# Optimization experiments

Hardware: AMD Instinct MI355X
Metric: run time of the kernel (lower is better)

## Reference

```python
import jax, jax.numpy as jnp
import numpy as np

N_RAYS = 8192
N_SAMPLES = 512  # hardcoded n_samples=512 in source
HID = 32
BOOSTER = 1.0


def setup_inputs() -> dict:
    key = jax.random.key(0)
    ks = jax.random.split(key, 8)
    # camera placed outside the box at z=-3, rays pointing toward +z into the aabb
    o = jnp.array([0.0, 0.0, -3.0]) + 0.05 * jax.random.normal(ks[0], (N_RAYS, 3))
    dxy = 0.5 * (2.0 * jax.random.uniform(ks[1], (N_RAYS, 2)) - 1.0)
    d = jnp.concatenate([dxy, jnp.ones((N_RAYS, 1))], axis=-1)  # unnormalized world dirs
    aabb = jnp.array([[-1.0, -1.0, -1.0], [1.0, 1.0, 1.0]])
    u = jax.random.uniform(ks[2], (N_RAYS, N_SAMPLES))  # stratified jitter
    W1 = 0.5 * jax.random.normal(ks[3], (3, HID))
    b1 = jnp.zeros((HID,))
    Wc = 0.2 * jax.random.normal(ks[4], (HID, 3))
    bc = jnp.zeros((3,))
    Wd = 0.2 * jax.random.normal(ks[5], (HID, 1))
    bd = jnp.zeros((1,))
    return dict(o=o, d=d, aabb=aabb, u=u, W1=W1, b1=b1, Wc=Wc, bc=bc, Wd=Wd, bd=bd)


def reference(o, d, aabb, u, W1, b1, Wc, bc, Wd, bd):
    # --- intersect_aabb (slab test) ---
    t1 = (aabb[0] - o) / d
    t2 = (aabb[1] - o) / d
    tnear = jnp.maximum(jnp.max(jnp.minimum(t1, t2), axis=-1), 0.0)  # [N]
    tfar = jnp.min(jnp.maximum(t1, t2), axis=-1)                      # [N]
    active = tnear < tfar                                             # [N] active_mask
    dnorm = jnp.linalg.norm(d, axis=-1, keepdims=True)                # [N,1]

    # --- sample_ray_step_stratified: T bins in [tnear, tfar], jittered ---
    idx = jnp.arange(N_SAMPLES, dtype=o.dtype)
    ts = tnear[:, None] + (tfar - tnear)[:, None] * (idx[None, :] + u) / N_SAMPLES  # [N,T]

    # --- query radiance field at xyz = o + d*ts ---
    xyz = o[:, None, :] + d[:, None, :] * ts[..., None]               # [N,T,3]
    ndc = 2.0 * (xyz - aabb[0]) / (aabb[1] - aabb[0]) - 1.0           # box-normalized
    inbox = jnp.all(jnp.abs(ndc) <= 1.0, axis=-1)                     # BoundsFilter.test
    h = jax.nn.relu(ndc @ W1 + b1)                                    # [N,T,HID]
    color = jax.nn.sigmoid(h @ Wc + bc)                               # [N,T,3]
    density = jax.nn.softplus(h @ Wd + bd)[..., 0]                    # [N,T]
    # masked scatter-back: out-of-box samples contribute zero
    density = jnp.where(inbox, density, 0.0)
    color = jnp.where(inbox[..., None], color, 0.0)

    # --- integrate_timesteps: alpha compositing with cumulative transmittance ---
    t_ext = jnp.concatenate([ts, (tfar + BOOSTER)[:, None]], axis=-1)
    delta = (t_ext[:, 1:] - t_ext[:, :-1]) * dnorm                    # [N,T]
    sd = density * delta
    trans = jnp.exp(-jnp.concatenate([jnp.zeros_like(sd[:, :1]), jnp.cumsum(sd[:, :-1], axis=-1)], axis=-1))
    w = trans * (1.0 - jnp.exp(-sd))                                  # weights [N,T]

    out_color = jnp.einsum('nt,ntc->nc', w, color)                    # color_map
    out_alpha = jnp.sum(w, axis=-1, keepdims=True)                    # alpha_map

    act = active[:, None].astype(o.dtype)                             # scatter to active rays only
    return jnp.concatenate([out_color * act, out_alpha * act], axis=-1)  # [N,4]
```

## Files before the change

### kernel.cpp

```cpp
#include <hip/hip_runtime.h>
#include <math.h>

#define NRAYS 8192
#define NS 512
#define HID 32
#define SPL 8

typedef float f32x2 __attribute__((ext_vector_type(2)));

__global__ __launch_bounds__(256) void render_kernel(
    const float* __restrict__ o_, const float* __restrict__ d_,
    const float* __restrict__ aabb, const float* __restrict__ u_,
    const float* __restrict__ W1, const float* __restrict__ b1,
    const float* __restrict__ Wc, const float* __restrict__ bc,
    const float* __restrict__ Wd, const float* __restrict__ bd,
    float* __restrict__ out)
{
    __shared__ float wsh[272];
    const int tid = threadIdx.x;

    if (tid < HID) {
        const int j = tid, p = j >> 1, h = j & 1;
        float* base = wsh + p * 16;
        base[0 + h]  = W1[0 * HID + j];
        base[2 + h]  = W1[1 * HID + j];
        base[4 + h]  = W1[2 * HID + j];
        base[6 + h]  = b1[j];
        base[8 + h]  = Wc[j * 3 + 0];
        base[10 + h] = Wc[j * 3 + 1];
        base[12 + h] = Wc[j * 3 + 2];
        base[14 + h] = Wd[j];
    } else if (tid == HID) {
        wsh[256] = bc[0]; wsh[257] = bc[1]; wsh[258] = bc[2]; wsh[259] = bd[0];
    }
    __syncthreads();

    const int lane = tid & 63;
    const int ray  = (blockIdx.x << 2) + (tid >> 6);
    if (ray >= NRAYS) return;

    const float ox = o_[ray * 3 + 0], oy = o_[ray * 3 + 1], oz = o_[ray * 3 + 2];
    const float dx = d_[ray * 3 + 0], dy = d_[ray * 3 + 1], dz = d_[ray * 3 + 2];
    const float lox = aabb[0], loy = aabb[1], loz = aabb[2];
    const float hix = aabb[3], hiy = aabb[4], hiz = aabb[5];

    float t1 = (lox - ox) / dx, t2 = (hix - ox) / dx;
    float tnear = fminf(t1, t2), tfar = fmaxf(t1, t2);
    t1 = (loy - oy) / dy; t2 = (hiy - oy) / dy;
    tnear = fmaxf(tnear, fminf(t1, t2)); tfar = fminf(tfar, fmaxf(t1, t2));
    t1 = (loz - oz) / dz; t2 = (hiz - oz) / dz;
    tnear = fmaxf(tnear, fminf(t1, t2)); tfar = fminf(tfar, fmaxf(t1, t2));
    tnear = fmaxf(tnear, 0.0f);

    float4 res = make_float4(0.0f, 0.0f, 0.0f, 0.0f);

    if (tnear < tfar) {
        const float dnorm = sqrtf(dx * dx + dy * dy + dz * dz);
        const float dt = (tfar - tnear) * (1.0f / (float)NS);
        const float sx = 2.0f / (hix - lox);
        const float sy = 2.0f / (hiy - loy);
        const float sz = 2.0f / (hiz - loz);
        const float bc0 = wsh[256], bc1 = wsh[257], bc2 = wsh[258], bd0 = wsh[259];

        const int base_t = lane * SPL;
        const float* __restrict__ urow = u_ + (size_t)ray * NS + base_t;
        const float4 uaq = *reinterpret_cast<const float4*>(urow);
        const float4 ubq = *reinterpret_cast<const float4*>(urow + 4);
        float us[9];
        us[0] = uaq.x; us[1] = uaq.y; us[2] = uaq.z; us[3] = uaq.w;
        us[4] = ubq.x; us[5] = ubq.y; us[6] = ubq.z; us[7] = ubq.w;
        us[8] = __shfl_down(uaq.x, 1);

        f32x2 nx2[SPL], ny2[SPL], nz2[SPL];
        float delta[SPL];
        #pragma unroll
        for (int s = 0; s < SPL; ++s) {
            const int t = base_t + s;
            const float ts = fmaf(dt, (float)t + us[s], tnear);
            float dl;
            if (t == NS - 1) dl = (tfar + 1.0f) - ts;
            else             dl = dt * (1.0f + us[s + 1] - us[s]);
            delta[s] = dl * dnorm;
            const float px = fmaf(dx, ts, ox);
            const float py = fmaf(dy, ts, oy);
            const float pz = fmaf(dz, ts, oz);
            const float nx = (px - lox) * sx - 1.0f;
            const float ny = (py - loy) * sy - 1.0f;
            const float nz = (pz - loz) * sz - 1.0f;
            nx2[s] = (f32x2){nx, nx};
            ny2[s] = (f32x2){ny, ny};
            nz2[s] = (f32x2){nz, nz};
        }

        f32x2 cr2[SPL], cg2[SPL], cb2[SPL], dd2[SPL];
        #pragma unroll
        for (int s = 0; s < SPL; ++s) {
            cr2[s] = (f32x2){bc0, 0.0f};
            cg2[s] = (f32x2){bc1, 0.0f};
            cb2[s] = (f32x2){bc2, 0.0f};
            dd2[s] = (f32x2){bd0, 0.0f};
        }
        const float4* __restrict__ wq = reinterpret_cast<const float4*>(wsh);
        #pragma unroll 4
        for (int p = 0; p < HID / 2; ++p) {
            const float4 q0 = wq[p * 4 + 0];
            const float4 q1 = wq[p * 4 + 1];
            const float4 q2 = wq[p * 4 + 2];
            const float4 q3 = wq[p * 4 + 3];
            const f32x2 w1x = {q0.x, q0.y}, w1y = {q0.z, q0.w};
            const f32x2 w1z = {q1.x, q1.y}, b12 = {q1.z, q1.w};
            const f32x2 wcr = {q2.x, q2.y}, wcg = {q2.z, q2.w};
            const f32x2 wcb = {q3.x, q3.y}, wd2 = {q3.z, q3.w};
            #pragma unroll
            for (int s = 0; s < SPL; ++s) {
                f32x2 h2 = __builtin_elementwise_fma(nx2[s], w1x,
                           __builtin_elementwise_fma(ny2[s], w1y,
                           __builtin_elementwise_fma(nz2[s], w1z, b12)));
                h2 = __builtin_elementwise_max(h2, (f32x2){0.0f, 0.0f});
                cr2[s] = __builtin_elementwise_fma(h2, wcr, cr2[s]);
                cg2[s] = __builtin_elementwise_fma(h2, wcg, cg2[s]);
                cb2[s] = __builtin_elementwise_fma(h2, wcb, cb2[s]);
                dd2[s] = __builtin_elementwise_fma(h2, wd2, dd2[s]);
            }
        }

        float sd[SPL], csum[SPL];
        float cum = 0.0f;
        #pragma unroll
        for (int s = 0; s < SPL; ++s) {
            const float dd = dd2[s].x + dd2[s].y;
            float dens = fmaxf(dd, 0.0f) + __logf(1.0f + __expf(-fabsf(dd)));
            const bool inbox = (fabsf(nx2[s].x) <= 1.0f) &&
                               (fabsf(ny2[s].x) <= 1.0f) &&
                               (fabsf(nz2[s].x) <= 1.0f);
            dens = inbox ? dens : 0.0f;
            sd[s] = dens * delta[s];
            cum += sd[s];
            csum[s] = cum;
        }

        float L = cum;
        #pragma unroll
        for (int off = 1; off < 64; off <<= 1) {
            const float v = __shfl_up(L, off);
            L += (lane >= off) ? v : 0.0f;
        }
        const float E = L - cum;

        float accR = 0.0f, accG = 0.0f, accB = 0.0f, accA = 0.0f;
        #pragma unroll
        for (int s = 0; s < SPL; ++s) {
            const float Ci = E + csum[s];
            const float Ce = Ci - sd[s];
            const float w = __expf(-Ce) - __expf(-Ci);
            const float cr = cr2[s].x + cr2[s].y;
            const float cg = cg2[s].x + cg2[s].y;
            const float cb = cb2[s].x + cb2[s].y;
            const float colR = __builtin_amdgcn_rcpf(1.0f + __expf(-cr));
            const float colG = __builtin_amdgcn_rcpf(1.0f + __expf(-cg));
            const float colB = __builtin_amdgcn_rcpf(1.0f + __expf(-cb));
            accR = fmaf(w, colR, accR);
            accG = fmaf(w, colG, accG);
            accB = fmaf(w, colB, accB);
            accA += w;
        }

        #pragma unroll
        for (int off = 32; off; off >>= 1) {
            accR += __shfl_xor(accR, off);
            accG += __shfl_xor(accG, off);
            accB += __shfl_xor(accB, off);
            accA += __shfl_xor(accA, off);
        }
        res = make_float4(accR, accG, accB, accA);
    }

    if (lane == 0) {
        reinterpret_cast<float4*>(out)[ray] = res;
    }
}

extern "C" void kernel_launch(void* const* d_in, const int* in_sizes, int n_in,
                              void* d_out, int out_size, void* d_ws, size_t ws_size,
                              hipStream_t stream) {
    const float* o_   = (const float*)d_in[0];
    const float* d_   = (const float*)d_in[1];
    const float* aabb = (const float*)d_in[2];
    const float* u_   = (const float*)d_in[3];
    const float* W1   = (const float*)d_in[4];
    const float* b1   = (const float*)d_in[5];
    const float* Wc   = (const float*)d_in[6];
    const float* bc   = (const float*)d_in[7];
    const float* Wd   = (const float*)d_in[8];
    const float* bd   = (const float*)d_in[9];
    float* out = (float*)d_out;

    render_kernel<<<NRAYS / 4, 256, 0, stream>>>(o_, d_, aabb, u_, W1, b1, Wc, bc, Wd, bd, out);
}
```

Measured before the change: 115.8 us.

## Fold first MLP layer into affine function of ts and telescope transmittance exps

The first-layer pre-activation is precomputed per hidden pair as A + ts*B, since normalized position is affine in ts. This drops the inner loop from three FMAs to one per pair. The per-sample in-box test is removed on the grounds that all samples lie between tnear and tfar. The weight computation now reuses the previous exponential, which halves the exps, and alpha comes from the telescoping sum. Samples near the box edge could round differently from the reference's in-box filter, and weights now come from differences of consecutive exponentials rather than computed independently.

```diff
diff --git a/kernel.cpp b/kernel.cpp
--- a/kernel.cpp
+++ b/kernel.cpp
@@ -62,6 +62,12 @@
         const float sz = 2.0f / (hiz - loz);
         const float bc0 = wsh[256], bc1 = wsh[257], bc2 = wsh[258], bd0 = wsh[259];
 
+        const float cx = (ox - lox) * sx - 1.0f, gx = dx * sx;
+        const float cy = (oy - loy) * sy - 1.0f, gy = dy * sy;
+        const float cz = (oz - loz) * sz - 1.0f, gz = dz * sz;
+        const f32x2 cx2 = {cx, cx}, cy2 = {cy, cy}, cz2 = {cz, cz};
+        const f32x2 gx2 = {gx, gx}, gy2 = {gy, gy}, gz2 = {gz, gz};
+
         const int base_t = lane * SPL;
         const float* __restrict__ urow = u_ + (size_t)ray * NS + base_t;
         const float4 uaq = *reinterpret_cast<const float4*>(urow);
@@ -71,25 +77,15 @@
         us[4] = ubq.x; us[5] = ubq.y; us[6] = ubq.z; us[7] = ubq.w;
         us[8] = __shfl_down(uaq.x, 1);
 
-        f32x2 nx2[SPL], ny2[SPL], nz2[SPL];
-        float delta[SPL];
+        float tsv[SPL], delta[SPL];
         #pragma unroll
         for (int s = 0; s < SPL; ++s) {
             const int t = base_t + s;
-            const float ts = fmaf(dt, (float)t + us[s], tnear);
+            tsv[s] = fmaf(dt, (float)t + us[s], tnear);
             float dl;
-            if (t == NS - 1) dl = (tfar + 1.0f) - ts;
+            if (t == NS - 1) dl = (tfar + 1.0f) - tsv[s];
             else             dl = dt * (1.0f + us[s + 1] - us[s]);
             delta[s] = dl * dnorm;
-            const float px = fmaf(dx, ts, ox);
-            const float py = fmaf(dy, ts, oy);
-            const float pz = fmaf(dz, ts, oz);
-            const float nx = (px - lox) * sx - 1.0f;
-            const float ny = (py - loy) * sy - 1.0f;
-            const float nz = (pz - loz) * sz - 1.0f;
-            nx2[s] = (f32x2){nx, nx};
-            ny2[s] = (f32x2){ny, ny};
-            nz2[s] = (f32x2){nz, nz};
         }
 
         f32x2 cr2[SPL], cg2[SPL], cb2[SPL], dd2[SPL];
@@ -111,11 +107,15 @@
             const f32x2 w1z = {q1.x, q1.y}, b12 = {q1.z, q1.w};
             const f32x2 wcr = {q2.x, q2.y}, wcg = {q2.z, q2.w};
             const f32x2 wcb = {q3.x, q3.y}, wd2 = {q3.z, q3.w};
+            const f32x2 A2 = __builtin_elementwise_fma(cx2, w1x,
+                             __builtin_elementwise_fma(cy2, w1y,
+                             __builtin_elementwise_fma(cz2, w1z, b12)));
+            const f32x2 B2 = __builtin_elementwise_fma(gx2, w1x,
+                             __builtin_elementwise_fma(gy2, w1y, gz2 * w1z));
             #pragma unroll
             for (int s = 0; s < SPL; ++s) {
-                f32x2 h2 = __builtin_elementwise_fma(nx2[s], w1x,
-                           __builtin_elementwise_fma(ny2[s], w1y,
-                           __builtin_elementwise_fma(nz2[s], w1z, b12)));
+                const f32x2 ts2 = {tsv[s], tsv[s]};
+                f32x2 h2 = __builtin_elementwise_fma(ts2, B2, A2);
                 h2 = __builtin_elementwise_max(h2, (f32x2){0.0f, 0.0f});
                 cr2[s] = __builtin_elementwise_fma(h2, wcr, cr2[s]);
                 cg2[s] = __builtin_elementwise_fma(h2, wcg, cg2[s]);
@@ -129,11 +129,7 @@
         #pragma unroll
         for (int s = 0; s < SPL; ++s) {
             const float dd = dd2[s].x + dd2[s].y;
-            float dens = fmaxf(dd, 0.0f) + __logf(1.0f + __expf(-fabsf(dd)));
-            const bool inbox = (fabsf(nx2[s].x) <= 1.0f) &&
-                               (fabsf(ny2[s].x) <= 1.0f) &&
-                               (fabsf(nz2[s].x) <= 1.0f);
-            dens = inbox ? dens : 0.0f;
+            const float dens = fmaxf(dd, 0.0f) + __logf(1.0f + __expf(-fabsf(dd)));
             sd[s] = dens * delta[s];
             cum += sd[s];
             csum[s] = cum;
@@ -147,12 +143,14 @@
         }
         const float E = L - cum;
 
-        float accR = 0.0f, accG = 0.0f, accB = 0.0f, accA = 0.0f;
+        float accR = 0.0f, accG = 0.0f, accB = 0.0f;
+        const float e0 = __expf(-E);
+        float eprev = e0;
         #pragma unroll
         for (int s = 0; s < SPL; ++s) {
-            const float Ci = E + csum[s];
-            const float Ce = Ci - sd[s];
-            const float w = __expf(-Ce) - __expf(-Ci);
+            const float ecur = __expf(-(E + csum[s]));
+            const float w = eprev - ecur;
+            eprev = ecur;
             const float cr = cr2[s].x + cr2[s].y;
             const float cg = cg2[s].x + cg2[s].y;
             const float cb = cb2[s].x + cb2[s].y;
@@ -162,8 +160,8 @@
             accR = fmaf(w, colR, accR);
             accG = fmaf(w, colG, accG);
             accB = fmaf(w, colB, accB);
-            accA += w;
         }
+        float accA = e0 - eprev;
 
         #pragma unroll
         for (int off = 32; off; off >>= 1) {
```

Measured after the change: 108.6 us. -6.3%, faster.
